# Optimization experiments

Measured on AMD Instinct MI355X. Metric: run time of the kernel, lower is better.

The kernel has to match this reference:

```python
import jax, jax.numpy as jnp
import numpy as np

DIMS = 2048
VOCAB = 512
T = 8192


def setup_inputs() -> dict:
    key = jax.random.key(0)
    ks = jax.random.split(key, 22)

    def lin_w(k, out_f, in_f):
        b = 1.0 / np.sqrt(in_f)
        return jax.random.uniform(k, (out_f, in_f), jnp.float32, -b, b)

    def lin_b(k, out_f, in_f):
        b = 1.0 / np.sqrt(in_f)
        return jax.random.uniform(k, (out_f,), jnp.float32, -b, b)

    inp = {
        'tokens': jax.random.randint(ks[0], (T,), 0, VOCAB, dtype=jnp.int32),
        'Wx': lin_w(ks[1], DIMS, VOCAB), 'bx': lin_b(ks[2], DIMS, VOCAB),
        'Uf': lin_w(ks[3], DIMS, DIMS), 'buf': lin_b(ks[4], DIMS, DIMS),
        'Wf': lin_w(ks[5], DIMS, DIMS), 'bwf': lin_b(ks[6], DIMS, DIMS),
        'Ui': lin_w(ks[7], DIMS, DIMS), 'bui': lin_b(ks[8], DIMS, DIMS),
        'Wi': lin_w(ks[9], DIMS, DIMS), 'bwi': lin_b(ks[10], DIMS, DIMS),
        'Uc': lin_w(ks[11], DIMS, DIMS), 'buc': lin_b(ks[12], DIMS, DIMS),
        'Wc': lin_w(ks[13], DIMS, DIMS), 'bwc': lin_b(ks[14], DIMS, DIMS),
        'Uo': lin_w(ks[15], DIMS, DIMS), 'buo': lin_b(ks[16], DIMS, DIMS),
        'Wo': lin_w(ks[17], DIMS, DIMS), 'bwo': lin_b(ks[18], DIMS, DIMS),
        'V': lin_w(ks[19], VOCAB, DIMS), 'bv': lin_b(ks[20], VOCAB, DIMS),
    }
    return inp


def reference(tokens, Wx, bx, Uf, buf, Wf, bwf, Ui, bui, Wi, bwi,
              Uc, buc, Wc, bwc, Uo, buo, Wo, bwo, V, bv):
    # one_hot(idx) @ Wx.T + bx  ==  column gather of Wx  -> [T, dims]
    x_seq = Wx.T[tokens] + bx
    # input-conditioned gate pre-activations computed as batched GEMMs
    gf = x_seq @ Wf.T + bwf  # [T, dims]
    gi = x_seq @ Wi.T + bwi
    gc = x_seq @ Wc.T + bwc
    go = x_seq @ Wo.T + bwo

    def step(carry, xs):
        h, c = carry
        gft, git, gct, got = xs
        f_t = jax.nn.sigmoid(h @ Uf.T + buf + gft)
        i_t = jax.nn.sigmoid(h @ Ui.T + bui + git)
        c_new = jnp.tanh(h @ Uc.T + buc + gct)
        c_t = f_t * c + i_t * c_new
        o_t = jax.nn.sigmoid(h @ Uo.T + buo + got)
        h_t = o_t * jnp.tanh(c_t)
        return (h_t, c_t), h_t

    h0 = jnp.zeros((DIMS,), jnp.float32)
    c0 = jnp.zeros((DIMS,), jnp.float32)
    (_, _), hs = jax.lax.scan(step, (h0, c0), (gf, gi, gc, go))  # hs: [T, dims]
    y = jax.nn.log_softmax(hs @ V.T + bv, axis=-1)  # [T, vocab]
    return y
```

## Files before the change

### kernel.cpp

```cpp
#include <hip/hip_runtime.h>
#include <hip/hip_bf16.h>
#include <stdint.h>

#define T_SEQ 8192
#define DIMS  2048
#define VOCAB 512
#define GS    ((size_t)VOCAB * DIMS)

typedef unsigned short u16;
typedef unsigned int   uint32;
typedef unsigned long long u64;

__device__ __forceinline__ float lo2f(uint32 u) { return __uint_as_float(u << 16); }
__device__ __forceinline__ float hi2f(uint32 u) { return __uint_as_float(u & 0xffff0000u); }

__global__ __launch_bounds__(256) void k_build_x(const float* __restrict__ Wx,
                                                 const float* __restrict__ bx,
                                                 float* __restrict__ X) {
  int i = blockIdx.x * 256 + threadIdx.x;
  int v = i & (VOCAB - 1);
  int d = i >> 9;
  X[(size_t)v * DIMS + d] = Wx[i] + bx[d];
}

__global__ __launch_bounds__(256) void k_gate_gemm(const float* __restrict__ X,
                                                   const float* __restrict__ Wg,
                                                   const float* __restrict__ bw,
                                                   float* __restrict__ Gout,
                                                   int gate) {
  __shared__ float Xs[32][64];
  __shared__ float Ws[32][64];
  const int v0 = blockIdx.y * 64;
  const int j0 = blockIdx.x * 64;
  const int tid = threadIdx.x;
  const int tx = tid & 15, ty = tid >> 4;
  float acc[4][4] = {{0.f}};
  for (int k0 = 0; k0 < DIMS; k0 += 32) {
    const int r = tid >> 2, q = tid & 3;
    {
      const float* src = X + (size_t)(v0 + r) * DIMS + k0 + q * 8;
      float4 a = ((const float4*)src)[0];
      float4 b = ((const float4*)src)[1];
      Xs[q*8+0][r]=a.x; Xs[q*8+1][r]=a.y; Xs[q*8+2][r]=a.z; Xs[q*8+3][r]=a.w;
      Xs[q*8+4][r]=b.x; Xs[q*8+5][r]=b.y; Xs[q*8+6][r]=b.z; Xs[q*8+7][r]=b.w;
      const float* wsrc = Wg + (size_t)(j0 + r) * DIMS + k0 + q * 8;
      float4 c = ((const float4*)wsrc)[0];
      float4 e = ((const float4*)wsrc)[1];
      Ws[q*8+0][r]=c.x; Ws[q*8+1][r]=c.y; Ws[q*8+2][r]=c.z; Ws[q*8+3][r]=c.w;
      Ws[q*8+4][r]=e.x; Ws[q*8+5][r]=e.y; Ws[q*8+6][r]=e.z; Ws[q*8+7][r]=e.w;
    }
    __syncthreads();
    #pragma unroll
    for (int k = 0; k < 32; ++k) {
      float xa[4], wb[4];
      *(float4*)xa = *(const float4*)&Xs[k][ty*4];
      *(float4*)wb = *(const float4*)&Ws[k][tx*4];
      #pragma unroll
      for (int a = 0; a < 4; ++a)
        #pragma unroll
        for (int b = 0; b < 4; ++b)
          acc[a][b] = fmaf(xa[a], wb[b], acc[a][b]);
    }
    __syncthreads();
  }
  #pragma unroll
  for (int a = 0; a < 4; ++a)
    #pragma unroll
    for (int b = 0; b < 4; ++b)
      Gout[(((size_t)(v0 + ty*4 + a) * DIMS + j0 + tx*4 + b) << 2) + gate] =
          acc[a][b] + bw[j0 + tx*4 + b];
}

template <typename HS> __device__ __forceinline__ void store_h4(HS* hs, size_t idx, float4 v);
template <> __device__ __forceinline__ void store_h4<float>(float* hs, size_t idx, float4 v) {
  *(float4*)(hs + idx) = v;
}
template <> __device__ __forceinline__ void store_h4<u16>(u16* hs, size_t idx, float4 v) {
  __hip_bfloat16 bx = __float2bfloat16(v.x);
  __hip_bfloat16 by = __float2bfloat16(v.y);
  __hip_bfloat16 bz = __float2bfloat16(v.z);
  __hip_bfloat16 bw = __float2bfloat16(v.w);
  ushort4 o;
  o.x = *reinterpret_cast<u16*>(&bx);
  o.y = *reinterpret_cast<u16*>(&by);
  o.z = *reinterpret_cast<u16*>(&bz);
  o.w = *reinterpret_cast<u16*>(&bw);
  *(ushort4*)(hs + idx) = o;
}

template <typename HS>
__global__ __launch_bounds__(512, 2) void k_lstm(
    const int* __restrict__ tokens,
    const float* __restrict__ G,
    uint32* hbuf,
    HS* __restrict__ hs,
    const float* __restrict__ Uf, const float* __restrict__ Ui,
    const float* __restrict__ Uc, const float* __restrict__ Uo,
    const float* __restrict__ bUf, const float* __restrict__ bUi,
    const float* __restrict__ bUc, const float* __restrict__ bUo) {
  __shared__ float4 h4[2][DIMS / 4];
  const int tid  = threadIdx.x;
  const int wave = tid >> 6;
  const int lane = tid & 63;
  const int gate = lane >> 4;
  const int sl   = lane & 15;
  const int jr   = blockIdx.x * 8 + wave;

  const float* Ug = (gate == 0) ? Uf : (gate == 1) ? Ui : (gate == 2) ? Uc : Uo;
  const float4* urow = (const float4*)(Ug + (size_t)jr * DIMS);
  float4 w[32];
  #pragma unroll
  for (int i = 0; i < 32; ++i) w[i] = urow[sl + 16 * i];
  #pragma unroll
  for (int i = 0; i < 32; ++i)
    asm volatile("" : "+v"(w[i].x), "+v"(w[i].y), "+v"(w[i].z), "+v"(w[i].w));

  float creg = 0.f, bias = 0.f, gvp = 0.f;
  if (sl == 0) {
    const float* Bg = (gate == 0) ? bUf : (gate == 1) ? bUi : (gate == 2) ? bUc : bUo;
    bias = Bg[jr];
    const int tok0 = tokens[0];
    gvp = G[((size_t)tok0 * DIMS + jr) * 4 + gate];
  }
  if (lane == 0) {
    __hip_atomic_store(&hbuf[jr], 0u, __ATOMIC_RELAXED, __HIP_MEMORY_SCOPE_AGENT);
    __hip_atomic_store(&hbuf[DIMS + jr], 0u, __ATOMIC_RELAXED, __HIP_MEMORY_SCOPE_AGENT);
  }

  #pragma unroll 1
  for (int t = 0; t < T_SEQ; ++t) {
    {
      const u64* hsrc = (const u64*)(hbuf + (size_t)(t & 1) * DIMS) + 2 * tid;
      const uint32 want = (uint32)t & 0xFFu;
      u64 u0 = __hip_atomic_load(hsrc + 0, __ATOMIC_RELAXED, __HIP_MEMORY_SCOPE_AGENT);
      u64 u1 = __hip_atomic_load(hsrc + 1, __ATOMIC_RELAXED, __HIP_MEMORY_SCOPE_AGENT);
      for (;;) {
        const bool ok0 = ((((uint32)u0 ^ want) | ((uint32)(u0 >> 32) ^ want)) & 0xFFu) == 0u;
        const bool ok1 = ((((uint32)u1 ^ want) | ((uint32)(u1 >> 32) ^ want)) & 0xFFu) == 0u;
        if (ok0 && ok1) break;
        if (!ok0) u0 = __hip_atomic_load(hsrc + 0, __ATOMIC_RELAXED, __HIP_MEMORY_SCOPE_AGENT);
        if (!ok1) u1 = __hip_atomic_load(hsrc + 1, __ATOMIC_RELAXED, __HIP_MEMORY_SCOPE_AGENT);
      }
      h4[t & 1][tid] = make_float4(__uint_as_float((uint32)u0),
                                   __uint_as_float((uint32)(u0 >> 32)),
                                   __uint_as_float((uint32)u1),
                                   __uint_as_float((uint32)(u1 >> 32)));
    }
    __syncthreads();
    if ((int)blockIdx.x == (t & 255)) {
      float4 hv4 = h4[t & 1][tid];
      store_h4<HS>(hs, (size_t)t * DIMS + 4 * (size_t)tid, hv4);
    }
    const float4* hb = h4[t & 1];
    float4 a4 = make_float4(0.f, 0.f, 0.f, 0.f);
    #pragma unroll
    for (int i = 0; i < 32; ++i) {
      float4 hv = hb[sl + 16 * i];
      a4.x = fmaf(w[i].x, hv.x, a4.x);
      a4.y = fmaf(w[i].y, hv.y, a4.y);
      a4.z = fmaf(w[i].z, hv.z, a4.z);
      a4.w = fmaf(w[i].w, hv.w, a4.w);
    }
    float acc = (a4.x + a4.y) + (a4.z + a4.w);
    #pragma unroll
    for (int d = 1; d <= 8; d <<= 1) acc += __shfl_xor(acc, d, 64);
    float act = 0.f;
    if (sl == 0) {
      const float y = acc + bias + gvp;
      const float s = 1.f / (1.f + __expf((gate == 2) ? (-2.f * y) : (-y)));
      act = (gate == 2) ? (2.f * s - 1.f) : s;
    }
    const float aI = __shfl(act, 16, 64);
    const float aC = __shfl(act, 32, 64);
    const float aO = __shfl(act, 48, 64);
    if (lane == 0) {
      creg = act * creg + aI * aC;
      const float th = 1.f - 2.f / (1.f + __expf(2.f * creg));
      const float hv = aO * th;
      const uint32 tb = (__float_as_uint(hv) & 0xFFFFFF00u) | ((uint32)(t + 1) & 0xFFu);
      __hip_atomic_store(&hbuf[(size_t)((t + 1) & 1) * DIMS + jr], tb,
                         __ATOMIC_RELAXED, __HIP_MEMORY_SCOPE_AGENT);
    }
    if (sl == 0) {
      const int tn = (t + 1 < T_SEQ) ? t + 1 : T_SEQ - 1;
      gvp = G[((size_t)tokens[tn] * DIMS + jr) * 4 + gate];
    }
  }
}

template <typename HS> __device__ __forceinline__ void load8(const HS* p, float* o);
template <> __device__ __forceinline__ void load8<float>(const float* p, float* o) {
  float4 a = ((const float4*)p)[0], b = ((const float4*)p)[1];
  o[0]=a.x; o[1]=a.y; o[2]=a.z; o[3]=a.w; o[4]=b.x; o[5]=b.y; o[6]=b.z; o[7]=b.w;
}
template <> __device__ __forceinline__ void load8<u16>(const u16* p, float* o) {
  uint4 u = *(const uint4*)p;
  o[0]=lo2f(u.x); o[1]=hi2f(u.x); o[2]=lo2f(u.y); o[3]=hi2f(u.y);
  o[4]=lo2f(u.z); o[5]=hi2f(u.z); o[6]=lo2f(u.w); o[7]=hi2f(u.w);
}

template <typename HS>
__global__ __launch_bounds__(256) void k_out_gemm(const HS* __restrict__ hs,
                                                  const float* __restrict__ V,
                                                  const float* __restrict__ bvb,
                                                  float* __restrict__ logits) {
  __shared__ float As[32][64];
  __shared__ float Bs[32][128];
  const int t0 = blockIdx.x * 64;
  const int v0 = blockIdx.y * 128;
  const int tid = threadIdx.x;
  const int tx = tid & 15, ty = tid >> 4;
  float acc[4][8] = {{0.f}};
  for (int k0 = 0; k0 < DIMS; k0 += 32) {
    {
      const int r = tid >> 2, q = tid & 3;
      float o8[8];
      load8<HS>(hs + (size_t)(t0 + r) * DIMS + k0 + q * 8, o8);
      #pragma unroll
      for (int s = 0; s < 8; ++s) As[q*8+s][r] = o8[s];
      const int rb = tid >> 1, c0 = (tid & 1) * 2;
      #pragma unroll
      for (int c = 0; c < 2; ++c) {
        float p8[8];
        load8<float>(V + (size_t)(v0 + rb) * DIMS + k0 + (c0 + c) * 8, p8);
        #pragma unroll
        for (int s = 0; s < 8; ++s) Bs[(c0+c)*8+s][rb] = p8[s];
      }
    }
    __syncthreads();
    #pragma unroll
    for (int k = 0; k < 32; ++k) {
      float av[4], bw8[8];
      *(float4*)av = *(const float4*)&As[k][ty*4];
      *(float4*)&bw8[0] = *(const float4*)&Bs[k][tx*8];
      *(float4*)&bw8[4] = *(const float4*)&Bs[k][tx*8+4];
      #pragma unroll
      for (int a = 0; a < 4; ++a)
        #pragma unroll
        for (int b = 0; b < 8; ++b)
          acc[a][b] = fmaf(av[a], bw8[b], acc[a][b]);
    }
    __syncthreads();
  }
  #pragma unroll
  for (int a = 0; a < 4; ++a)
    #pragma unroll
    for (int b = 0; b < 8; ++b)
      logits[(size_t)(t0 + ty*4 + a) * VOCAB + v0 + tx*8 + b] =
          acc[a][b] + bvb[v0 + tx*8 + b];
}

__global__ __launch_bounds__(256) void k_logsoftmax(float* __restrict__ logits) {
  const int t = blockIdx.x;
  const int tid = threadIdx.x;
  float* row = logits + (size_t)t * VOCAB;
  float x0 = row[tid], x1 = row[tid + 256];
  float m = fmaxf(x0, x1);
  #pragma unroll
  for (int d = 32; d; d >>= 1) m = fmaxf(m, __shfl_xor(m, d, 64));
  __shared__ float r1[4], r2[4];
  if ((tid & 63) == 0) r1[tid >> 6] = m;
  __syncthreads();
  m = fmaxf(fmaxf(r1[0], r1[1]), fmaxf(r1[2], r1[3]));
  float s = __expf(x0 - m) + __expf(x1 - m);
  #pragma unroll
  for (int d = 32; d; d >>= 1) s += __shfl_xor(s, d, 64);
  if ((tid & 63) == 0) r2[tid >> 6] = s;
  __syncthreads();
  s = r2[0] + r2[1] + r2[2] + r2[3];
  const float lse = m + __logf(s);
  row[tid] = x0 - lse;
  row[tid + 256] = x1 - lse;
}

extern "C" void kernel_launch(void* const* d_in, const int* in_sizes, int n_in,
                              void* d_out, int out_size, void* d_ws, size_t ws_size,
                              hipStream_t stream) {
  const int*   tokens = (const int*)d_in[0];
  const float* Wx  = (const float*)d_in[1];
  const float* bx  = (const float*)d_in[2];
  const float* Uf  = (const float*)d_in[3];
  const float* bUf = (const float*)d_in[4];
  const float* Wf  = (const float*)d_in[5];
  const float* bwf = (const float*)d_in[6];
  const float* Ui  = (const float*)d_in[7];
  const float* bUi = (const float*)d_in[8];
  const float* Wi  = (const float*)d_in[9];
  const float* bwi = (const float*)d_in[10];
  const float* Uc  = (const float*)d_in[11];
  const float* bUc = (const float*)d_in[12];
  const float* Wc  = (const float*)d_in[13];
  const float* bwc = (const float*)d_in[14];
  const float* Uo  = (const float*)d_in[15];
  const float* bUo = (const float*)d_in[16];
  const float* Wo  = (const float*)d_in[17];
  const float* bwo = (const float*)d_in[18];
  const float* V   = (const float*)d_in[19];
  const float* bv  = (const float*)d_in[20];

  char* ws = (char*)d_ws;
  float* X = (float*)ws;
  float* G = (float*)(ws + 4194304ull);
  uint32* hbuf = (uint32*)(ws + 20971520ull);
  char* rest = ws + 21004288ull;
  const bool f32path = ws_size >= 88113152ull;

  k_build_x<<<dim3((DIMS * VOCAB) / 256), dim3(256), 0, stream>>>(Wx, bx, X);
  dim3 gg(DIMS / 64, VOCAB / 64);
  k_gate_gemm<<<gg, dim3(256), 0, stream>>>(X, Wf, bwf, G, 0);
  k_gate_gemm<<<gg, dim3(256), 0, stream>>>(X, Wi, bwi, G, 1);
  k_gate_gemm<<<gg, dim3(256), 0, stream>>>(X, Wc, bwc, G, 2);
  k_gate_gemm<<<gg, dim3(256), 0, stream>>>(X, Wo, bwo, G, 3);

  float* logits = (float*)d_out;
  if (f32path) {
    float* hs = (float*)rest;
    k_lstm<float><<<dim3(256), dim3(512), 0, stream>>>(
        tokens, G, hbuf, hs, Uf, Ui, Uc, Uo, bUf, bUi, bUc, bUo);
    k_out_gemm<float><<<dim3(T_SEQ / 64, VOCAB / 128), dim3(256), 0, stream>>>(
        hs, V, bv, logits);
  } else {
    u16* hs = (u16*)rest;
    k_lstm<u16><<<dim3(256), dim3(512), 0, stream>>>(
        tokens, G, hbuf, hs, Uf, Ui, Uc, Uo, bUf, bUi, bUc, bUo);
    k_out_gemm<u16><<<dim3(T_SEQ / 64, VOCAB / 128), dim3(256), 0, stream>>>(
        hs, V, bv, logits);
  }
  k_logsoftmax<<<dim3(T_SEQ), dim3(256), 0, stream>>>(logits);
}
```

Baseline: 19.48 ms.

## Compute all four LSTM gates per lane and reduce with DPP row shifts

The recurrent kernel is remapped so every lane holds weights for all four gates over eight float4 chunks of one hidden row, instead of one gate over 32 chunks per 16-lane group. Each h value read from LDS now feeds four gate accumulators, cutting LDS reads per step. The cross-lane reduction uses DPP row_shr adds plus two xor shuffles, and lane 15 computes all four activations and the cell update itself, with the gate bias and G values fetched as one float4. In exchange, four accumulators are reduced instead of one, and the activation exponentials run serially in a single lane on the per-step critical path.

```diff
diff --git a/kernel.cpp b/kernel.cpp
--- a/kernel.cpp
+++ b/kernel.cpp
@@ -13,6 +13,10 @@
 
 __device__ __forceinline__ float lo2f(uint32 u) { return __uint_as_float(u << 16); }
 __device__ __forceinline__ float hi2f(uint32 u) { return __uint_as_float(u & 0xffff0000u); }
+
+#define ROW_SHR_ADD(x, N)                                                          \
+  x += __int_as_float(__builtin_amdgcn_update_dpp(                                 \
+      0, __float_as_int(x), 0x110 + (N), 0xF, 0xF, true))
 
 __global__ __launch_bounds__(256) void k_build_x(const float* __restrict__ Wx,
                                                  const float* __restrict__ bx,
@@ -102,25 +106,33 @@
   const int tid  = threadIdx.x;
   const int wave = tid >> 6;
   const int lane = tid & 63;
-  const int gate = lane >> 4;
-  const int sl   = lane & 15;
   const int jr   = blockIdx.x * 8 + wave;
 
-  const float* Ug = (gate == 0) ? Uf : (gate == 1) ? Ui : (gate == 2) ? Uc : Uo;
-  const float4* urow = (const float4*)(Ug + (size_t)jr * DIMS);
-  float4 w[32];
-  #pragma unroll
-  for (int i = 0; i < 32; ++i) w[i] = urow[sl + 16 * i];
-  #pragma unroll
-  for (int i = 0; i < 32; ++i)
-    asm volatile("" : "+v"(w[i].x), "+v"(w[i].y), "+v"(w[i].z), "+v"(w[i].w));
-
-  float creg = 0.f, bias = 0.f, gvp = 0.f;
-  if (sl == 0) {
-    const float* Bg = (gate == 0) ? bUf : (gate == 1) ? bUi : (gate == 2) ? bUc : bUo;
-    bias = Bg[jr];
-    const int tok0 = tokens[0];
-    gvp = G[((size_t)tok0 * DIMS + jr) * 4 + gate];
+  float4 w4[4][8];
+  {
+    const float4* r0 = (const float4*)(Uf + (size_t)jr * DIMS);
+    const float4* r1 = (const float4*)(Ui + (size_t)jr * DIMS);
+    const float4* r2 = (const float4*)(Uc + (size_t)jr * DIMS);
+    const float4* r3 = (const float4*)(Uo + (size_t)jr * DIMS);
+    #pragma unroll
+    for (int i = 0; i < 8; ++i) {
+      w4[0][i] = r0[lane + 64 * i];
+      w4[1][i] = r1[lane + 64 * i];
+      w4[2][i] = r2[lane + 64 * i];
+      w4[3][i] = r3[lane + 64 * i];
+    }
+  }
+  #pragma unroll
+  for (int g = 0; g < 4; ++g)
+    #pragma unroll
+    for (int i = 0; i < 8; ++i)
+      asm volatile("" : "+v"(w4[g][i].x), "+v"(w4[g][i].y), "+v"(w4[g][i].z), "+v"(w4[g][i].w));
+
+  float creg = 0.f, bF = 0.f, bI = 0.f, bC = 0.f, bO = 0.f;
+  float4 gv = make_float4(0.f, 0.f, 0.f, 0.f);
+  if (lane == 15) {
+    bF = bUf[jr]; bI = bUi[jr]; bC = bUc[jr]; bO = bUo[jr];
+    gv = ((const float4*)G)[(size_t)tokens[0] * DIMS + jr];
   }
   if (lane == 0) {
     __hip_atomic_store(&hbuf[jr], 0u, __ATOMIC_RELAXED, __HIP_MEMORY_SCOPE_AGENT);
@@ -152,38 +164,44 @@
       store_h4<HS>(hs, (size_t)t * DIMS + 4 * (size_t)tid, hv4);
     }
     const float4* hb = h4[t & 1];
-    float4 a4 = make_float4(0.f, 0.f, 0.f, 0.f);
-    #pragma unroll
-    for (int i = 0; i < 32; ++i) {
-      float4 hv = hb[sl + 16 * i];
-      a4.x = fmaf(w[i].x, hv.x, a4.x);
-      a4.y = fmaf(w[i].y, hv.y, a4.y);
-      a4.z = fmaf(w[i].z, hv.z, a4.z);
-      a4.w = fmaf(w[i].w, hv.w, a4.w);
-    }
-    float acc = (a4.x + a4.y) + (a4.z + a4.w);
-    #pragma unroll
-    for (int d = 1; d <= 8; d <<= 1) acc += __shfl_xor(acc, d, 64);
-    float act = 0.f;
-    if (sl == 0) {
-      const float y = acc + bias + gvp;
-      const float s = 1.f / (1.f + __expf((gate == 2) ? (-2.f * y) : (-y)));
-      act = (gate == 2) ? (2.f * s - 1.f) : s;
-    }
-    const float aI = __shfl(act, 16, 64);
-    const float aC = __shfl(act, 32, 64);
-    const float aO = __shfl(act, 48, 64);
-    if (lane == 0) {
-      creg = act * creg + aI * aC;
+    float a0 = 0.f, a1 = 0.f, a2 = 0.f, a3 = 0.f;
+    #pragma unroll
+    for (int i = 0; i < 8; ++i) {
+      float4 hv = hb[lane + 64 * i];
+      a0 = fmaf(w4[0][i].x, hv.x, a0); a0 = fmaf(w4[0][i].y, hv.y, a0);
+      a0 = fmaf(w4[0][i].z, hv.z, a0); a0 = fmaf(w4[0][i].w, hv.w, a0);
+      a1 = fmaf(w4[1][i].x, hv.x, a1); a1 = fmaf(w4[1][i].y, hv.y, a1);
+      a1 = fmaf(w4[1][i].z, hv.z, a1); a1 = fmaf(w4[1][i].w, hv.w, a1);
+      a2 = fmaf(w4[2][i].x, hv.x, a2); a2 = fmaf(w4[2][i].y, hv.y, a2);
+      a2 = fmaf(w4[2][i].z, hv.z, a2); a2 = fmaf(w4[2][i].w, hv.w, a2);
+      a3 = fmaf(w4[3][i].x, hv.x, a3); a3 = fmaf(w4[3][i].y, hv.y, a3);
+      a3 = fmaf(w4[3][i].z, hv.z, a3); a3 = fmaf(w4[3][i].w, hv.w, a3);
+    }
+    ROW_SHR_ADD(a0, 1); ROW_SHR_ADD(a1, 1); ROW_SHR_ADD(a2, 1); ROW_SHR_ADD(a3, 1);
+    ROW_SHR_ADD(a0, 2); ROW_SHR_ADD(a1, 2); ROW_SHR_ADD(a2, 2); ROW_SHR_ADD(a3, 2);
+    ROW_SHR_ADD(a0, 4); ROW_SHR_ADD(a1, 4); ROW_SHR_ADD(a2, 4); ROW_SHR_ADD(a3, 4);
+    ROW_SHR_ADD(a0, 8); ROW_SHR_ADD(a1, 8); ROW_SHR_ADD(a2, 8); ROW_SHR_ADD(a3, 8);
+    a0 += __shfl_xor(a0, 16, 64); a1 += __shfl_xor(a1, 16, 64);
+    a2 += __shfl_xor(a2, 16, 64); a3 += __shfl_xor(a3, 16, 64);
+    a0 += __shfl_xor(a0, 32, 64); a1 += __shfl_xor(a1, 32, 64);
+    a2 += __shfl_xor(a2, 32, 64); a3 += __shfl_xor(a3, 32, 64);
+    if (lane == 15) {
+      const float yf = a0 + bF + gv.x;
+      const float yi = a1 + bI + gv.y;
+      const float yc = a2 + bC + gv.z;
+      const float yo = a3 + bO + gv.w;
+      const float fg = 1.f / (1.f + __expf(-yf));
+      const float ig = 1.f / (1.f + __expf(-yi));
+      const float cn = 1.f - 2.f / (1.f + __expf(2.f * yc));
+      const float og = 1.f / (1.f + __expf(-yo));
+      creg = fg * creg + ig * cn;
       const float th = 1.f - 2.f / (1.f + __expf(2.f * creg));
-      const float hv = aO * th;
+      const float hv = og * th;
       const uint32 tb = (__float_as_uint(hv) & 0xFFFFFF00u) | ((uint32)(t + 1) & 0xFFu);
       __hip_atomic_store(&hbuf[(size_t)((t + 1) & 1) * DIMS + jr], tb,
                          __ATOMIC_RELAXED, __HIP_MEMORY_SCOPE_AGENT);
-    }
-    if (sl == 0) {
       const int tn = (t + 1 < T_SEQ) ? t + 1 : T_SEQ - 1;
-      gvp = G[((size_t)tokens[tn] * DIMS + jr) * 4 + gate];
+      gv = ((const float4*)G)[(size_t)tokens[tn] * DIMS + jr];
     }
   }
 }
```

Result: slower. 27.58 ms (+41.6%).
